# Kernel tuning notes

Hardware: AMD Instinct MI355X
Metric: run time of the kernel (lower is better)

## Reference

```python
import jax, jax.numpy as jnp
import numpy as np

B, T, M, D, K, L = 128, 50, 4, 64, 64, 16  # batch, seq len, num_beh, embed dim, num_classes, capsule_length
NUM_ITEMS = 100000
R_ITERS = 3


def _dyn_gru(x, C, Wx, bx, Wh, bh):
    """Dynamic capsule GRU. x: [B,M,T,D], C: [B,M,T,K,L] (routing state modulates update gate).
    Returns final hidden beh_e [B,M,K,L] and per-step candidate states beh_N [B,M,T,K,L]."""
    # precompute input projections for all steps: [B,M,T,3,K,L]
    gi = (jnp.einsum('bmtd,mdg->bmtg', x, Wx) + bx[:, None, :]).reshape(x.shape[0], M, T, 3, K, L)

    def step(h, inp):
        gi_t, C_t = inp  # gi_t: [B,M,3,K,L], C_t: [B,M,K,L]
        gh = (jnp.einsum('bmkl,mklg->bmkg', h, Wh) + bh).reshape(h.shape[0], M, K, 3, L)
        r = jax.nn.sigmoid(gi_t[:, :, 0] + gh[:, :, :, 0])
        z = jax.nn.sigmoid(gi_t[:, :, 1] + gh[:, :, :, 1] + C_t)  # dynamic gate via routing state C
        n = jnp.tanh(gi_t[:, :, 2] + r * gh[:, :, :, 2])
        h_new = (1.0 - z) * n + z * h
        return h_new, n

    h0 = jnp.zeros((x.shape[0], M, K, L), x.dtype)
    h_fin, ns = jax.lax.scan(step, h0, (jnp.moveaxis(gi, 2, 0), jnp.moveaxis(C, 2, 0)))
    return h_fin, jnp.moveaxis(ns, 0, 2)


def setup_inputs() -> dict:
    key = jax.random.key(0)
    ks = jax.random.split(key, 9)
    names = ['purchase_seq', 'cart_seq', 'fav_seq', 'click_seq']
    seqs = {n: jax.random.randint(k, (B, T), 0, NUM_ITEMS + 1) for n, k in zip(names, ks[:4])}
    item_emb = jax.random.normal(ks[4], (NUM_ITEMS + 1, D), jnp.float32) * 0.02
    item_emb = item_emb.at[0].set(0.0)  # padding_idx=0
    W = 0.01 * jax.random.uniform(ks[5], (K, L, M, K), jnp.float32)
    W_coef = 0.1 * jax.random.normal(ks[6], (K, D + L, L), jnp.float32)
    alpha = jnp.ones((1,), jnp.float32) * K
    w = jnp.ones((K,), jnp.float32)
    bias = jnp.zeros((K,), jnp.float32)
    gru_Wx = 0.05 * jax.random.normal(ks[7], (M, D, 3 * K * L), jnp.float32)
    gru_bx = jnp.zeros((M, 3 * K * L), jnp.float32)
    gru_Wh = 0.05 * jax.random.normal(ks[8], (M, K, L, 3 * L), jnp.float32)
    gru_bh = jnp.zeros((M, K, 3 * L), jnp.float32)
    return dict(**seqs, item_emb=item_emb, W=W, W_coef=W_coef, alpha=alpha, w=w, bias=bias,
                gru_Wx=gru_Wx, gru_bx=gru_bx, gru_Wh=gru_Wh, gru_bh=gru_bh)


def reference(purchase_seq, cart_seq, fav_seq, click_seq, item_emb, W, W_coef,
              alpha, w, bias, gru_Wx, gru_bx, gru_Wh, gru_bh):
    sg = jax.lax.stop_gradient

    def embed(seq):
        mask = (seq != 0).astype(item_emb.dtype)[..., None]
        return item_emb[seq] * mask

    x = jnp.stack([embed(purchase_seq), embed(cart_seq), embed(fav_seq), embed(click_seq)], axis=1)  # [B,M,T,D]
    bsz = x.shape[0]
    b = jnp.zeros((bsz, K, K, 1), x.dtype)
    C = jnp.zeros((bsz, M, T, K, L), x.dtype)

    # routing iterations (all GRU outputs / W / alpha / w / bias / item_emb detached; W_coef live)
    for _ in range(R_ITERS - 1):
        beh_e, beh_N = _dyn_gru(sg(x), sg(C), sg(gru_Wx), sg(gru_bx), sg(gru_Wh), sg(gru_bh))
        beh_e = sg(beh_e).transpose(0, 2, 1, 3)  # [B,K,M,L]
        u = jnp.einsum('bctd,cdtC->bcCd', beh_e, sg(W))  # [B,K,K,L]
        c = jax.nn.softmax(b, axis=2)
        v = sg(alpha) * jnp.sum(c * u, axis=1)  # [B,K,L]
        v_ = jnp.linalg.norm(v, axis=-1) * sg(w) + sg(bias)  # [B,K]
        E = sg(item_emb)
        p = jax.nn.softmax(v_ @ E.T, axis=-1) @ E  # [B,D]
        p = jnp.broadcast_to(p[:, None, :], (bsz, K, D))
        r = jnp.einsum('bcd,cdD->bcD', jnp.concatenate([p, v], axis=-1), W_coef)  # [B,K,L]
        b = b + jnp.sum(u * r[:, None], axis=-1, keepdims=True)
        C = C + sg(beh_N) * r[:, None, None]

    beh_e, _ = _dyn_gru(x, C, gru_Wx, gru_bx, gru_Wh, gru_bh)
    beh_e = beh_e.transpose(0, 2, 1, 3)
    u_hat = jnp.einsum('bctd,cdtC->bcCd', beh_e, W)
    c = jax.nn.softmax(b, axis=2)
    v = alpha * jnp.sum(c * u_hat, axis=1)
    v_ = jnp.linalg.norm(v, axis=-1) * w + bias
    return v_ @ item_emb.T  # [B, num_items+1]
```

## Files before the change

kernel.cpp:

```cpp
#include <hip/hip_runtime.h>
#include <hip/hip_bf16.h>
#include <cstdint>
#include <cstddef>

#define B_   128
#define T_   50
#define M_   4
#define D_   64
#define K_   64
#define L_   16
#define NIT  100001
#define NBP3 256
#define CHUNK3 391
#define PSTRIDE 8320

typedef unsigned short u16;
typedef unsigned int   u32;
typedef __attribute__((ext_vector_type(8))) short short8;
typedef __attribute__((ext_vector_type(4))) short short4v;
typedef __attribute__((ext_vector_type(4))) float f32x4;

__device__ __forceinline__ float bf2f(u16 v){ u32 u = ((u32)v)<<16; float f; __builtin_memcpy(&f,&u,4); return f; }
__device__ __forceinline__ u16 f2bf(float f){
  u32 u; __builtin_memcpy(&u,&f,4);
  u32 r = (u + 0x7FFFu + ((u>>16)&1u)) >> 16;
  return (u16)r;
}
__device__ __forceinline__ float fexp(float x){ return __builtin_amdgcn_exp2f(x*1.4426950408889634f); }
__device__ __forceinline__ float fsig(float x){ return __builtin_amdgcn_rcpf(1.0f + fexp(-x)); }
__device__ __forceinline__ float ftanh(float x){ return 1.0f - 2.0f*__builtin_amdgcn_rcpf(1.0f + fexp(2.0f*x)); }
__device__ __forceinline__ void unpack8(const u32* s, short8& h, short8& l){
  #pragma unroll
  for (int q=0;q<8;q++){ h[q]=(short)(s[q]&0xFFFFu); l[q]=(short)(s[q]>>16); }
}

#define MFMA32(A,Bv,C) __builtin_amdgcn_mfma_f32_16x16x32_bf16(A,Bv,C,0,0,0)

#if __has_builtin(__builtin_amdgcn_mfma_f32_16x16x16bf16_1k)
__device__ __forceinline__ f32x4 mfma16(short4v a, short4v b, f32x4 c){
  return __builtin_amdgcn_mfma_f32_16x16x16bf16_1k(a,b,c,0,0,0);
}
#elif __has_builtin(__builtin_amdgcn_mfma_f32_16x16x16_bf16)
__device__ __forceinline__ f32x4 mfma16(short4v a, short4v b, f32x4 c){
  return __builtin_amdgcn_mfma_f32_16x16x16_bf16(a,b,c,0,0,0);
}
#else
__device__ __forceinline__ f32x4 mfma16(short4v a, short4v b, f32x4 c){
  asm("v_mfma_f32_16x16x16_bf16 %0, %1, %2, %0" : "+v"(c) : "v"(a), "v"(b));
  return c;
}
#endif

__global__ __launch_bounds__(256) void k_prep_x(const int* __restrict__ s0, const int* __restrict__ s1,
  const int* __restrict__ s2, const int* __restrict__ s3, const float* __restrict__ E,
  u16* __restrict__ xh, u16* __restrict__ xl)
{
  int id = blockIdx.x*256 + threadIdx.x;
  int e8 = id & 7;
  int rm = id >> 3;
  int m = rm / 6400; int r = rm - m*6400;
  int t = r >> 7, b = r & 127;
  const int* sq = (m==0)? s0 : (m==1)? s1 : (m==2)? s2 : s3;
  int idx = sq[b*T_ + t];
  float sc = (idx==0)? 0.0f : 1.0f;
  const float4* ep = (const float4*)(E + (size_t)idx*64 + e8*8);
  float4 v0 = ep[0], v1 = ep[1];
  float vals[8] = {v0.x,v0.y,v0.z,v0.w,v1.x,v1.y,v1.z,v1.w};
  u32 hw[4], lw[4];
  #pragma unroll
  for (int q=0;q<4;q++){
    float f0 = vals[2*q]*sc, f1 = vals[2*q+1]*sc;
    u16 h0 = f2bf(f0), h1 = f2bf(f1);
    u16 l0 = f2bf(f0 - bf2f(h0)), l1 = f2bf(f1 - bf2f(h1));
    hw[q] = (u32)h0 | ((u32)h1<<16);
    lw[q] = (u32)l0 | ((u32)l1<<16);
  }
  size_t off = (size_t)rm*64 + e8*8;
  uint4 hv; hv.x=hw[0]; hv.y=hw[1]; hv.z=hw[2]; hv.w=hw[3];
  uint4 lv; lv.x=lw[0]; lv.y=lw[1]; lv.z=lw[2]; lv.w=lw[3];
  *(uint4*)(xh + off) = hv;
  *(uint4*)(xl + off) = lv;
}

__global__ __launch_bounds__(256) void k_prep_w(const float* __restrict__ Wx,
  u16* __restrict__ wh, u16* __restrict__ wl)
{
  __shared__ float tl[64][65];
  int m = blockIdx.x / 48, gt = blockIdx.x % 48;
  for (int it=0; it<16; ++it){
    int li = threadIdx.x + it*256;
    int dl = li >> 6, gl = li & 63;
    tl[dl][gl] = Wx[((size_t)m*64 + dl)*3072 + gt*64 + gl];
  }
  __syncthreads();
  for (int it=0; it<2; ++it){
    int unit = threadIdx.x + it*256;
    int gl = unit >> 3, d8 = unit & 7;
    u32 hw[4], lw[4];
    #pragma unroll
    for (int q=0;q<4;q++){
      float f0 = tl[d8*8+2*q][gl], f1 = tl[d8*8+2*q+1][gl];
      u16 h0 = f2bf(f0), h1 = f2bf(f1);
      u16 l0 = f2bf(f0 - bf2f(h0)), l1 = f2bf(f1 - bf2f(h1));
      hw[q] = (u32)h0 | ((u32)h1<<16);
      lw[q] = (u32)l0 | ((u32)l1<<16);
    }
    size_t off = ((size_t)m*3072 + gt*64 + gl)*64 + d8*8;
    uint4 hv; hv.x=hw[0]; hv.y=hw[1]; hv.z=hw[2]; hv.w=hw[3];
    uint4 lv; lv.x=lw[0]; lv.y=lw[1]; lv.z=lw[2]; lv.w=lw[3];
    *(uint4*)(wh + off) = hv;
    *(uint4*)(wl + off) = lv;
  }
}

template<int PASS>
__global__ __launch_bounds__(256,2) void k_gru_mfma(
  const u16* __restrict__ xh, const u16* __restrict__ xl,
  const u16* __restrict__ wh, const u16* __restrict__ wl,
  const float* __restrict__ Wh, const float* __restrict__ bx, const float* __restrict__ bhp,
  const float* __restrict__ rp1, const float* __restrict__ rp2,
  const u16* __restrict__ Nr1, const u16* __restrict__ Nr2,
  u16* __restrict__ Nw, float* __restrict__ behE)
{
  int tid = threadIdx.x;
  int lane = tid & 63;
  int n16 = lane & 15, quad = lane >> 4;
  int j0 = quad*4;
  int wid = blockIdx.x*4 + (tid>>6);
  int bt = wid & 7, k = (wid>>3)&63, m = wid>>9;
  int b = bt*16 + n16;

  short8 WxH[3][2], WxL[3][2];
  #pragma unroll
  for (int g=0; g<3; ++g){
    int grow = g*1024 + k*16 + n16;
    #pragma unroll
    for (int c=0; c<2; ++c){
      size_t off = ((size_t)(m*3072 + grow))*64 + c*32 + quad*8;
      WxH[g][c] = *(const short8*)(wh + off);
      WxL[g][c] = *(const short8*)(wl + off);
    }
  }
  const float* whp = Wh + ((size_t)(m*64+k)*16)*48;
  short4v WhH[3], WhL[3];
  #pragma unroll
  for (int g=0; g<3; ++g){
    short4v hhv, llv;
    #pragma unroll
    for (int i=0;i<4;i++){
      float w = whp[(j0+i)*48 + g*16 + n16];
      u16 hbits = f2bf(w);
      hhv[i] = (short)hbits;
      llv[i] = (short)f2bf(w - bf2f(hbits));
    }
    WhH[g]=hhv; WhL[g]=llv;
  }
  float biasv[3][4], bhn[4];
  #pragma unroll
  for (int g=0; g<3; ++g)
    #pragma unroll
    for (int rg=0; rg<4; ++rg){
      int j = j0+rg;
      float tb = bx[m*3072 + g*1024 + k*16 + j];
      if (g<2) tb += bhp[(m*64+k)*48 + g*16 + j];
      biasv[g][rg] = tb;
    }
  #pragma unroll
  for (int rg=0; rg<4; ++rg) bhn[rg] = bhp[(m*64+k)*48 + 32 + j0 + rg];

  float rv1[4]={0.f,0.f,0.f,0.f}, rv2[4]={0.f,0.f,0.f,0.f};
  if (PASS>=2){
    float4 q = *(const float4*)(rp1 + ((size_t)b*64+k)*16 + j0);
    rv1[0]=q.x; rv1[1]=q.y; rv1[2]=q.z; rv1[3]=q.w;
  }
  if (PASS==3){
    float4 q = *(const float4*)(rp2 + ((size_t)b*64+k)*16 + j0);
    rv2[0]=q.x; rv2[1]=q.y; rv2[2]=q.z; rv2[3]=q.w;
  }

  size_t xrow  = ((size_t)m*6400 + bt*16 + n16)*64 + quad*8;
  size_t nbase = ((size_t)(m*64+k))*102400 + (size_t)b*16 + j0;

  short4v hH = {0,0,0,0}, hL = {0,0,0,0};
  float hprev[4] = {0.f,0.f,0.f,0.f};

  short8 A0,A1,A2,A3, Bb0,Bb1,Bb2,Bb3;
  uint2 AN1={0,0}, AN2={0,0}, BN1={0,0}, BN2={0,0};

#define LOADA(tt) { size_t xo = xrow + (size_t)(tt)*8192; \
  A0 = *(const short8*)(xh + xo); A1 = *(const short8*)(xh + xo + 32); \
  A2 = *(const short8*)(xl + xo); A3 = *(const short8*)(xl + xo + 32); \
  if (PASS>=2) AN1 = *(const uint2*)(Nr1 + nbase + (size_t)(tt)*2048); \
  if (PASS==3) AN2 = *(const uint2*)(Nr2 + nbase + (size_t)(tt)*2048); }
#define LOADB(tt) { size_t xo = xrow + (size_t)(tt)*8192; \
  Bb0 = *(const short8*)(xh + xo); Bb1 = *(const short8*)(xh + xo + 32); \
  Bb2 = *(const short8*)(xl + xo); Bb3 = *(const short8*)(xl + xo + 32); \
  if (PASS>=2) BN1 = *(const uint2*)(Nr1 + nbase + (size_t)(tt)*2048); \
  if (PASS==3) BN2 = *(const uint2*)(Nr2 + nbase + (size_t)(tt)*2048); }

#define GRU_STEP(tt, X0,X1,X2,X3, NV1, NV2) { \
  f32x4 giA0 = {biasv[0][0], biasv[0][1], biasv[0][2], biasv[0][3]}; \
  f32x4 giA1 = {biasv[1][0], biasv[1][1], biasv[1][2], biasv[1][3]}; \
  f32x4 giA2 = {biasv[2][0], biasv[2][1], biasv[2][2], biasv[2][3]}; \
  giA0 = MFMA32(WxH[0][0], X0, giA0); giA1 = MFMA32(WxH[1][0], X0, giA1); giA2 = MFMA32(WxH[2][0], X0, giA2); \
  giA0 = MFMA32(WxH[0][1], X1, giA0); giA1 = MFMA32(WxH[1][1], X1, giA1); giA2 = MFMA32(WxH[2][1], X1, giA2); \
  giA0 = MFMA32(WxL[0][0], X0, giA0); giA1 = MFMA32(WxL[1][0], X0, giA1); giA2 = MFMA32(WxL[2][0], X0, giA2); \
  giA0 = MFMA32(WxL[0][1], X1, giA0); giA1 = MFMA32(WxL[1][1], X1, giA1); giA2 = MFMA32(WxL[2][1], X1, giA2); \
  giA0 = MFMA32(WxH[0][0], X2, giA0); giA1 = MFMA32(WxH[1][0], X2, giA1); giA2 = MFMA32(WxH[2][0], X2, giA2); \
  giA0 = MFMA32(WxH[0][1], X3, giA0); giA1 = MFMA32(WxH[1][1], X3, giA1); giA2 = MFMA32(WxH[2][1], X3, giA2); \
  f32x4 ghr = {0.f,0.f,0.f,0.f}, ghz = {0.f,0.f,0.f,0.f}; \
  f32x4 ghn = {bhn[0], bhn[1], bhn[2], bhn[3]}; \
  ghr = mfma16(WhH[0], hH, ghr); ghz = mfma16(WhH[1], hH, ghz); ghn = mfma16(WhH[2], hH, ghn); \
  ghr = mfma16(WhL[0], hH, ghr); ghz = mfma16(WhL[1], hH, ghz); ghn = mfma16(WhL[2], hH, ghn); \
  ghr = mfma16(WhH[0], hL, ghr); ghz = mfma16(WhH[1], hL, ghz); ghn = mfma16(WhH[2], hL, ghn); \
  u32 np0=0, np1=0; \
  short4v hHn = {0,0,0,0}, hLn = {0,0,0,0}; \
  _Pragma("unroll") \
  for (int rg=0; rg<4; ++rg){ \
    float Ct = 0.f; \
    if (PASS>=2){ u32 wb = (rg<2)? NV1.x : NV1.y; Ct = bf2f((u16)(wb >> ((rg&1)*16))) * rv1[rg]; } \
    if (PASS==3){ u32 wb = (rg<2)? NV2.x : NV2.y; Ct += bf2f((u16)(wb >> ((rg&1)*16))) * rv2[rg]; } \
    float rr = fsig(giA0[rg] + ghr[rg]); \
    float zz = fsig(giA1[rg] + ghz[rg] + Ct); \
    float nn = ftanh(giA2[rg] + rr*ghn[rg]); \
    float hvv = nn + zz*(hprev[rg]-nn); \
    hprev[rg] = hvv; \
    if (PASS<=2){ \
      u32 nb = f2bf(nn); \
      if (rg==0) np0 |= nb; else if (rg==1) np0 |= nb<<16; else if (rg==2) np1 |= nb; else np1 |= nb<<16; \
    } \
    u16 hb = f2bf(hvv); \
    hHn[rg] = (short)hb; \
    hLn[rg] = (short)f2bf(hvv - bf2f(hb)); \
  } \
  if (PASS<=2){ uint2 stv; stv.x=np0; stv.y=np1; *(uint2*)(Nw + nbase + (size_t)(tt)*2048) = stv; } \
  hH = hHn; hL = hLn; \
}

  LOADA(0);
  for (int t=0; t<48; t+=2){
    LOADB(t+1);
    GRU_STEP(t,   A0,A1,A2,A3, AN1,AN2);
    LOADA(t+2);
    GRU_STEP(t+1, Bb0,Bb1,Bb2,Bb3, BN1,BN2);
  }
  LOADB(49);
  GRU_STEP(48, A0,A1,A2,A3, AN1,AN2);
  GRU_STEP(49, Bb0,Bb1,Bb2,Bb3, BN1,BN2);
#undef GRU_STEP
#undef LOADA
#undef LOADB

  float4 stv; stv.x=hprev[0]; stv.y=hprev[1]; stv.z=hprev[2]; stv.w=hprev[3];
  *(float4*)(behE + (((size_t)b*64 + k)*4 + m)*16 + j0) = stv;
}

__global__ __launch_bounds__(256) void k_cv(const float* __restrict__ bmat, const float* __restrict__ behE,
  const float* __restrict__ W, const float* __restrict__ alpha, const float* __restrict__ wv,
  const float* __restrict__ bias, float* __restrict__ vout, float* __restrict__ vT)
{
  __shared__ float cm[64][65];
  __shared__ float vsh[64][17];
  __shared__ float besh[4096];
  int b = blockIdx.x, tid = threadIdx.x;
  for (int it=0; it<16; ++it){
    int li = tid + it*256;
    cm[li>>6][li&63] = bmat[(size_t)b*4096 + li];
    besh[li] = behE[(size_t)b*4096 + li];
  }
  __syncthreads();
  if (tid < 64){
    float mx = -1e30f;
    for (int jj=0;jj<64;jj++) mx = fmaxf(mx, cm[tid][jj]);
    float sm = 0.f;
    for (int jj=0;jj<64;jj++){ float e = fexp(cm[tid][jj]-mx); cm[tid][jj]=e; sm+=e; }
    float inv = 1.0f/sm;
    for (int jj=0;jj<64;jj++) cm[tid][jj] *= inv;
  }
  __syncthreads();
  int j = tid & 63, dq = tid>>6;
  float a0=0,a1=0,a2=0,a3=0;
  for (int i=0;i<64;++i){
    float cij = cm[i][j];
    #pragma unroll
    for (int q=0;q<4;++q){
      int d = dq*4+q;
      const float* wp = W + ((size_t)((i*16+d)*4))*64 + j;
      float uu = besh[i*64+d]*wp[0] + besh[i*64+16+d]*wp[64]
               + besh[i*64+32+d]*wp[128] + besh[i*64+48+d]*wp[192];
      float cu = cij*uu;
      if (q==0) a0 += cu; else if (q==1) a1 += cu; else if (q==2) a2 += cu; else a3 += cu;
    }
  }
  float al = alpha[0];
  a0*=al; a1*=al; a2*=al; a3*=al;
  vsh[j][dq*4]=a0; vsh[j][dq*4+1]=a1; vsh[j][dq*4+2]=a2; vsh[j][dq*4+3]=a3;
  float* vp = vout + ((size_t)b*64 + j)*16 + dq*4;
  vp[0]=a0; vp[1]=a1; vp[2]=a2; vp[3]=a3;
  __syncthreads();
  if (tid < 64){
    float s=0.f;
    #pragma unroll
    for (int dd=0; dd<16; ++dd){ float q = vsh[tid][dd]; s += q*q; }
    vT[tid*128 + b] = sqrtf(s)*wv[tid] + bias[tid];
  }
}

__global__ __launch_bounds__(256) void k_prep_v(const float* __restrict__ vT, u32* __restrict__ vBp)
{
  int id = blockIdx.x*256 + threadIdx.x;
  int b = id>>6, c = id&63;
  float v = vT[c*128 + b];
  u16 h = f2bf(v); u16 l = f2bf(v - bf2f(h));
  vBp[id] = (u32)h | ((u32)l<<16);
}

__global__ __launch_bounds__(256) void k_pfused(const u32* __restrict__ vBp, const float* __restrict__ E,
  float* __restrict__ partial)
{
  __shared__ u16 etAh[32*72], etAl[32*72];
  __shared__ u16 etBh[64*32], etBl[64*32];
  __shared__ u32 exT[128*36];
  int tid = threadIdx.x, lane = tid&63, w = tid>>6;
  int n16 = lane&15, quad = lane>>4;

  short8 vh[2][2], vl[2][2];
  #pragma unroll
  for (int nt2=0; nt2<2; ++nt2){
    int b = (2*w+nt2)*16 + n16;
    #pragma unroll
    for (int s=0; s<2; ++s){
      u32 tmp[8];
      const u32* src = vBp + b*64 + s*32 + quad*8;
      #pragma unroll
      for (int q=0;q<8;q++) tmp[q]=src[q];
      unpack8(tmp, vh[nt2][s], vl[nt2][s]);
    }
  }
  f32x4 pacc[2][4];
  #pragma unroll
  for (int a2=0;a2<2;a2++)
    #pragma unroll
    for (int b2=0;b2<4;b2++){ pacc[a2][b2][0]=0.f; pacc[a2][b2][1]=0.f; pacc[a2][b2][2]=0.f; pacc[a2][b2][3]=0.f; }
  float srun[2] = {0.f, 0.f};

  int start = blockIdx.x*CHUNK3;
  int bend = start + CHUNK3; if (bend > NIT) bend = NIT;
  int sitem = tid>>3, sc0 = (tid&7)*8;
  for (int ch=0; ch<13; ++ch){
    int i0 = start + ch*32;
    if (i0 >= bend) break;
    {
      int gidx = i0 + sitem;
      float vals[8];
      if (gidx < NIT){
        float4 a = ((const float4*)E)[(size_t)gidx*16 + (sc0>>2)];
        float4 b2 = ((const float4*)E)[(size_t)gidx*16 + (sc0>>2) + 1];
        vals[0]=a.x; vals[1]=a.y; vals[2]=a.z; vals[3]=a.w;
        vals[4]=b2.x; vals[5]=b2.y; vals[6]=b2.z; vals[7]=b2.w;
      } else {
        #pragma unroll
        for (int q=0;q<8;q++) vals[q]=0.f;
      }
      u16 hh[8], ll[8];
      #pragma unroll
      for (int q=0;q<8;q++){ hh[q]=f2bf(vals[q]); ll[q]=f2bf(vals[q]-bf2f(hh[q])); }
      *(short8*)(etAh + sitem*72 + sc0) = *(short8*)hh;
      *(short8*)(etAl + sitem*72 + sc0) = *(short8*)ll;
      #pragma unroll
      for (int q=0;q<8;q++){
        etBh[(sc0+q)*32 + sitem] = hh[q];
        etBl[(sc0+q)*32 + sitem] = ll[q];
      }
    }
    __syncthreads();
    short8 Eh[2][2], El[2][2];
    #pragma unroll
    for (int mt=0; mt<2; ++mt)
      #pragma unroll
      for (int s=0; s<2; ++s){
        Eh[mt][s] = *(const short8*)(etAh + (mt*16 + n16)*72 + s*32 + quad*8);
        El[mt][s] = *(const short8*)(etAl + (mt*16 + n16)*72 + s*32 + quad*8);
      }
    #pragma unroll
    for (int mt=0; mt<2; ++mt){
      #pragma unroll
      for (int nt2=0; nt2<2; ++nt2){
        f32x4 a = {0.f,0.f,0.f,0.f};
        #pragma unroll
        for (int s=0; s<2; ++s){
          a = __builtin_amdgcn_mfma_f32_16x16x32_bf16(Eh[mt][s], vh[nt2][s], a, 0,0,0);
          a = __builtin_amdgcn_mfma_f32_16x16x32_bf16(Eh[mt][s], vl[nt2][s], a, 0,0,0);
          a = __builtin_amdgcn_mfma_f32_16x16x32_bf16(El[mt][s], vh[nt2][s], a, 0,0,0);
        }
        u32 packed[4];
        #pragma unroll
        for (int rg=0; rg<4; ++rg){
          int it_g = i0 + mt*16 + quad*4 + rg;
          float ex = (it_g < bend)? fexp(a[rg]) : 0.f;
          srun[nt2] += ex;
          u16 h = f2bf(ex); u16 l = f2bf(ex - bf2f(h));
          packed[rg] = (u32)h | ((u32)l<<16);
        }
        int bl = (2*w+nt2)*16 + n16;
        uint4 st; st.x=packed[0]; st.y=packed[1]; st.z=packed[2]; st.w=packed[3];
        *(uint4*)(exT + bl*36 + mt*16 + quad*4) = st;
      }
    }
    __syncthreads();
    short8 Xh[2], Xl[2];
    #pragma unroll
    for (int mt2=0; mt2<2; ++mt2){
      int bl = (2*w+mt2)*16 + n16;
      uint4 t0 = *(const uint4*)(exT + bl*36 + quad*8);
      uint4 t1 = *(const uint4*)(exT + bl*36 + quad*8 + 4);
      u32 tmp[8] = {t0.x,t0.y,t0.z,t0.w,t1.x,t1.y,t1.z,t1.w};
      unpack8(tmp, Xh[mt2], Xl[mt2]);
    }
    #pragma unroll
    for (int nt3=0; nt3<4; ++nt3){
      int d = nt3*16 + n16;
      short8 Bh = *(const short8*)(etBh + d*32 + quad*8);
      short8 Bl = *(const short8*)(etBl + d*32 + quad*8);
      #pragma unroll
      for (int mt2=0; mt2<2; ++mt2){
        pacc[mt2][nt3] = __builtin_amdgcn_mfma_f32_16x16x32_bf16(Xh[mt2], Bh, pacc[mt2][nt3], 0,0,0);
        pacc[mt2][nt3] = __builtin_amdgcn_mfma_f32_16x16x32_bf16(Xh[mt2], Bl, pacc[mt2][nt3], 0,0,0);
        pacc[mt2][nt3] = __builtin_amdgcn_mfma_f32_16x16x32_bf16(Xl[mt2], Bh, pacc[mt2][nt3], 0,0,0);
      }
    }
    __syncthreads();
  }
  float* dst = partial + (size_t)blockIdx.x*PSTRIDE;
  #pragma unroll
  for (int mt2=0; mt2<2; ++mt2)
    #pragma unroll
    for (int nt3=0; nt3<4; ++nt3)
      #pragma unroll
      for (int rg=0; rg<4; ++rg){
        int b_g = (2*w+mt2)*16 + quad*4 + rg;
        int d_g = nt3*16 + n16;
        dst[b_g*64 + d_g] = pacc[mt2][nt3][rg];
      }
  #pragma unroll
  for (int nt2=0; nt2<2; ++nt2){
    float vsum = srun[nt2];
    vsum += __shfl_xor(vsum, 16);
    vsum += __shfl_xor(vsum, 32);
    if (quad == 0) dst[8192 + (2*w+nt2)*16 + n16] = vsum;
  }
}

__global__ __launch_bounds__(256) void k_pcomb(const float* __restrict__ partial, float* __restrict__ p)
{
  int id = blockIdx.x*256 + threadIdx.x;
  int b = id>>6;
  float a = 0.f, s = 0.f;
  for (int q=0;q<NBP3;q++){
    a += partial[(size_t)q*PSTRIDE + id];
    s += partial[(size_t)q*PSTRIDE + 8192 + b];
  }
  p[id] = a/s;
}

__global__ __launch_bounds__(256) void k_r(const float* __restrict__ p, const float* __restrict__ v,
  const float* __restrict__ Wc, float* __restrict__ r, float* __restrict__ rT)
{
  int gid = blockIdx.x*256 + threadIdx.x;
  int l = gid & 15, j = (gid>>4)&63, b = gid>>10;
  const float* wc = Wc + ((size_t)j*80)*16 + l;
  const float* pbp = p + b*64;
  float acc = 0.f;
  #pragma unroll 8
  for (int d=0; d<64; ++d) acc += pbp[d]*wc[d*16];
  const float* vb = v + ((size_t)b*64 + j)*16;
  #pragma unroll
  for (int d=0; d<16; ++d) acc += vb[d]*wc[(64+d)*16];
  r[((size_t)b*64+j)*16 + l] = acc;
  rT[((size_t)b*16+l)*64 + j] = acc;
}

__global__ __launch_bounds__(256) void k_bupd(const float* __restrict__ behE, const float* __restrict__ W,
  const float* __restrict__ rT, float* __restrict__ bmat)
{
  int lane = threadIdx.x & 63;
  int idx = blockIdx.x*4 + (threadIdx.x>>6);
  int b = idx >> 6, i = idx & 63;
  const float* be = behE + (size_t)idx*64;
  const float* rp = rT + (size_t)b*1024;
  float acc = 0.f;
  #pragma unroll
  for (int d=0; d<16; ++d){
    const float* wp = W + ((size_t)((i*16+d)*4))*64 + lane;
    float uu = be[d]*wp[0] + be[16+d]*wp[64] + be[32+d]*wp[128] + be[48+d]*wp[192];
    acc += uu * rp[d*64 + lane];
  }
  bmat[(size_t)idx*64 + lane] += acc;
}

__global__ __launch_bounds__(256) void k_logits(const u32* __restrict__ vBp, const float* __restrict__ E,
  float* __restrict__ out)
{
  __shared__ u16 etAh[64*72], etAl[64*72];
  __shared__ float lt[128*68];
  int tid = threadIdx.x, lane = tid&63, w = tid>>6;
  int n16 = lane&15, quad = lane>>4;
  short8 vh[2][2], vl[2][2];
  #pragma unroll
  for (int nt2=0; nt2<2; ++nt2){
    int b = (2*w+nt2)*16 + n16;
    #pragma unroll
    for (int s=0; s<2; ++s){
      u32 tmp[8];
      const u32* src = vBp + b*64 + s*32 + quad*8;
      #pragma unroll
      for (int q=0;q<8;q++) tmp[q]=src[q];
      unpack8(tmp, vh[nt2][s], vl[nt2][s]);
    }
  }
  int i0 = blockIdx.x*64;
  {
    int sitem = tid>>2, sc0 = (tid&3)*16;
    int gidx = i0 + sitem;
    float vals[16];
    if (gidx < NIT){
      #pragma unroll
      for (int q=0;q<4;q++){
        float4 a = ((const float4*)E)[(size_t)gidx*16 + (sc0>>2) + q];
        vals[4*q]=a.x; vals[4*q+1]=a.y; vals[4*q+2]=a.z; vals[4*q+3]=a.w;
      }
    } else {
      #pragma unroll
      for (int q=0;q<16;q++) vals[q]=0.f;
    }
    u16 hh[16], ll[16];
    #pragma unroll
    for (int q=0;q<16;q++){ hh[q]=f2bf(vals[q]); ll[q]=f2bf(vals[q]-bf2f(hh[q])); }
    *(short8*)(etAh + sitem*72 + sc0)     = *(short8*)hh;
    *(short8*)(etAh + sitem*72 + sc0 + 8) = *(short8*)(hh+8);
    *(short8*)(etAl + sitem*72 + sc0)     = *(short8*)ll;
    *(short8*)(etAl + sitem*72 + sc0 + 8) = *(short8*)(ll+8);
  }
  __syncthreads();
  #pragma unroll
  for (int mt=0; mt<4; ++mt){
    short8 Eh[2], El[2];
    #pragma unroll
    for (int s=0; s<2; ++s){
      Eh[s] = *(const short8*)(etAh + (mt*16 + n16)*72 + s*32 + quad*8);
      El[s] = *(const short8*)(etAl + (mt*16 + n16)*72 + s*32 + quad*8);
    }
    #pragma unroll
    for (int nt2=0; nt2<2; ++nt2){
      f32x4 a = {0.f,0.f,0.f,0.f};
      #pragma unroll
      for (int s=0; s<2; ++s){
        a = __builtin_amdgcn_mfma_f32_16x16x32_bf16(Eh[s], vh[nt2][s], a, 0,0,0);
        a = __builtin_amdgcn_mfma_f32_16x16x32_bf16(Eh[s], vl[nt2][s], a, 0,0,0);
        a = __builtin_amdgcn_mfma_f32_16x16x32_bf16(El[s], vh[nt2][s], a, 0,0,0);
      }
      int b = (2*w+nt2)*16 + n16;
      *(float4*)(lt + b*68 + mt*16 + quad*4) = *(float4*)&a;
    }
  }
  __syncthreads();
  int col = tid & 63, rgp = tid >> 6;
  if (i0 + col < NIT){
    #pragma unroll
    for (int rr=0; rr<32; ++rr){
      int b = rgp*32 + rr;
      out[(size_t)b*NIT + i0 + col] = lt[b*68 + col];
    }
  }
}

extern "C" void kernel_launch(void* const* d_in, const int* in_sizes, int n_in,
                              void* d_out, int out_size, void* d_ws, size_t ws_size,
                              hipStream_t stream)
{
  (void)in_sizes; (void)n_in; (void)out_size; (void)ws_size;
  const int*   s0 = (const int*)d_in[0];
  const int*   s1 = (const int*)d_in[1];
  const int*   s2 = (const int*)d_in[2];
  const int*   s3 = (const int*)d_in[3];
  const float* E  = (const float*)d_in[4];
  const float* W  = (const float*)d_in[5];
  const float* Wc = (const float*)d_in[6];
  const float* alpha = (const float*)d_in[7];
  const float* wv    = (const float*)d_in[8];
  const float* bias  = (const float*)d_in[9];
  const float* Wx = (const float*)d_in[10];
  const float* bx = (const float*)d_in[11];
  const float* Wh = (const float*)d_in[12];
  const float* bh = (const float*)d_in[13];

  char* ws = (char*)d_ws;
  size_t off = 0;
  auto alloc = [&](size_t bytes)->void*{ void* q = ws + off; off += (bytes + 255) & ~(size_t)255; return q; };
  u16*   N1   = (u16*)  alloc((size_t)M_*K_*T_*B_*16*2);
  u16*   N2   = (u16*)  alloc((size_t)M_*K_*T_*B_*16*2);
  u16*   xh   = (u16*)  alloc((size_t)M_*6400*64*2);
  u16*   xl   = (u16*)  alloc((size_t)M_*6400*64*2);
  u16*   wh   = (u16*)  alloc((size_t)M_*3072*64*2);
  u16*   wl   = (u16*)  alloc((size_t)M_*3072*64*2);
  float* bmat = (float*)alloc((size_t)B_*64*64*4);
  float* behE = (float*)alloc((size_t)B_*64*4*16*4);
  float* v    = (float*)alloc((size_t)B_*64*16*4);
  float* vT   = (float*)alloc((size_t)64*128*4);
  u32*   vBp  = (u32*)  alloc((size_t)128*64*4);
  float* r1   = (float*)alloc((size_t)B_*64*16*4);
  float* rT1  = (float*)alloc((size_t)B_*64*16*4);
  float* r2   = (float*)alloc((size_t)B_*64*16*4);
  float* rT2  = (float*)alloc((size_t)B_*64*16*4);
  float* p    = (float*)alloc((size_t)B_*64*4);
  float* partial = (float*)alloc((size_t)NBP3*PSTRIDE*4);

  hipMemsetAsync(bmat, 0, (size_t)B_*64*64*4, stream);
  k_prep_x<<<800,256,0,stream>>>(s0,s1,s2,s3,E,xh,xl);
  k_prep_w<<<192,256,0,stream>>>(Wx,wh,wl);

  k_gru_mfma<1><<<512,256,0,stream>>>(xh,xl,wh,wl,Wh,bx,bh,
                                      nullptr,nullptr,nullptr,nullptr, N1, behE);
  k_cv<<<128,256,0,stream>>>(bmat,behE,W,alpha,wv,bias,v,vT);
  k_prep_v<<<32,256,0,stream>>>(vT,vBp);
  k_pfused<<<NBP3,256,0,stream>>>(vBp,E,partial);
  k_pcomb<<<32,256,0,stream>>>(partial,p);
  k_r<<<512,256,0,stream>>>(p,v,Wc,r1,rT1);
  k_bupd<<<2048,256,0,stream>>>(behE,W,rT1,bmat);

  k_gru_mfma<2><<<512,256,0,stream>>>(xh,xl,wh,wl,Wh,bx,bh,
                                      r1,nullptr, N1,nullptr, N2, behE);
  k_cv<<<128,256,0,stream>>>(bmat,behE,W,alpha,wv,bias,v,vT);
  k_prep_v<<<32,256,0,stream>>>(vT,vBp);
  k_pfused<<<NBP3,256,0,stream>>>(vBp,E,partial);
  k_pcomb<<<32,256,0,stream>>>(partial,p);
  k_r<<<512,256,0,stream>>>(p,v,Wc,r2,rT2);
  k_bupd<<<2048,256,0,stream>>>(behE,W,rT2,bmat);

  k_gru_mfma<3><<<512,256,0,stream>>>(xh,xl,wh,wl,Wh,bx,bh,
                                      r1,r2, N1,N2, nullptr, behE);
  k_cv<<<128,256,0,stream>>>(bmat,behE,W,alpha,wv,bias,v,vT);
  k_prep_v<<<32,256,0,stream>>>(vT,vBp);
  k_logits<<<1563,256,0,stream>>>(vBp,E,(float*)d_out);
}
```

Measured before the change: 505.2 us.

## Software-pipeline GRU input projection one step ahead of recurrent update

Splits each GRU step into an input-projection stage (the Wx MFMAs on x_t) and a recurrent stage (the Wh MFMAs plus gate math). The projection for step t+1 is now issued before the recurrent update of step t, and loads run two steps ahead. Because the projection does not depend on the hidden state, its MFMAs can overlap the latency of the serial recurrent chain. The cost is more live accumulator registers, which may lower occupancy or cause spills.

```diff
diff --git a/kernel.cpp b/kernel.cpp
--- a/kernel.cpp
+++ b/kernel.cpp
@@ -184,72 +184,84 @@
   short4v hH = {0,0,0,0}, hL = {0,0,0,0};
   float hprev[4] = {0.f,0.f,0.f,0.f};
 
-  short8 A0,A1,A2,A3, Bb0,Bb1,Bb2,Bb3;
-  uint2 AN1={0,0}, AN2={0,0}, BN1={0,0}, BN2={0,0};
-
-#define LOADA(tt) { size_t xo = xrow + (size_t)(tt)*8192; \
-  A0 = *(const short8*)(xh + xo); A1 = *(const short8*)(xh + xo + 32); \
-  A2 = *(const short8*)(xl + xo); A3 = *(const short8*)(xl + xo + 32); \
-  if (PASS>=2) AN1 = *(const uint2*)(Nr1 + nbase + (size_t)(tt)*2048); \
-  if (PASS==3) AN2 = *(const uint2*)(Nr2 + nbase + (size_t)(tt)*2048); }
-#define LOADB(tt) { size_t xo = xrow + (size_t)(tt)*8192; \
-  Bb0 = *(const short8*)(xh + xo); Bb1 = *(const short8*)(xh + xo + 32); \
-  Bb2 = *(const short8*)(xl + xo); Bb3 = *(const short8*)(xl + xo + 32); \
-  if (PASS>=2) BN1 = *(const uint2*)(Nr1 + nbase + (size_t)(tt)*2048); \
-  if (PASS==3) BN2 = *(const uint2*)(Nr2 + nbase + (size_t)(tt)*2048); }
-
-#define GRU_STEP(tt, X0,X1,X2,X3, NV1, NV2) { \
-  f32x4 giA0 = {biasv[0][0], biasv[0][1], biasv[0][2], biasv[0][3]}; \
-  f32x4 giA1 = {biasv[1][0], biasv[1][1], biasv[1][2], biasv[1][3]}; \
-  f32x4 giA2 = {biasv[2][0], biasv[2][1], biasv[2][2], biasv[2][3]}; \
-  giA0 = MFMA32(WxH[0][0], X0, giA0); giA1 = MFMA32(WxH[1][0], X0, giA1); giA2 = MFMA32(WxH[2][0], X0, giA2); \
-  giA0 = MFMA32(WxH[0][1], X1, giA0); giA1 = MFMA32(WxH[1][1], X1, giA1); giA2 = MFMA32(WxH[2][1], X1, giA2); \
-  giA0 = MFMA32(WxL[0][0], X0, giA0); giA1 = MFMA32(WxL[1][0], X0, giA1); giA2 = MFMA32(WxL[2][0], X0, giA2); \
-  giA0 = MFMA32(WxL[0][1], X1, giA0); giA1 = MFMA32(WxL[1][1], X1, giA1); giA2 = MFMA32(WxL[2][1], X1, giA2); \
-  giA0 = MFMA32(WxH[0][0], X2, giA0); giA1 = MFMA32(WxH[1][0], X2, giA1); giA2 = MFMA32(WxH[2][0], X2, giA2); \
-  giA0 = MFMA32(WxH[0][1], X3, giA0); giA1 = MFMA32(WxH[1][1], X3, giA1); giA2 = MFMA32(WxH[2][1], X3, giA2); \
-  f32x4 ghr = {0.f,0.f,0.f,0.f}, ghz = {0.f,0.f,0.f,0.f}; \
-  f32x4 ghn = {bhn[0], bhn[1], bhn[2], bhn[3]}; \
-  ghr = mfma16(WhH[0], hH, ghr); ghz = mfma16(WhH[1], hH, ghz); ghn = mfma16(WhH[2], hH, ghn); \
-  ghr = mfma16(WhL[0], hH, ghr); ghz = mfma16(WhL[1], hH, ghz); ghn = mfma16(WhL[2], hH, ghn); \
-  ghr = mfma16(WhH[0], hL, ghr); ghz = mfma16(WhH[1], hL, ghz); ghn = mfma16(WhH[2], hL, ghn); \
-  u32 np0=0, np1=0; \
-  short4v hHn = {0,0,0,0}, hLn = {0,0,0,0}; \
-  _Pragma("unroll") \
-  for (int rg=0; rg<4; ++rg){ \
-    float Ct = 0.f; \
-    if (PASS>=2){ u32 wb = (rg<2)? NV1.x : NV1.y; Ct = bf2f((u16)(wb >> ((rg&1)*16))) * rv1[rg]; } \
-    if (PASS==3){ u32 wb = (rg<2)? NV2.x : NV2.y; Ct += bf2f((u16)(wb >> ((rg&1)*16))) * rv2[rg]; } \
-    float rr = fsig(giA0[rg] + ghr[rg]); \
-    float zz = fsig(giA1[rg] + ghz[rg] + Ct); \
-    float nn = ftanh(giA2[rg] + rr*ghn[rg]); \
-    float hvv = nn + zz*(hprev[rg]-nn); \
-    hprev[rg] = hvv; \
-    if (PASS<=2){ \
-      u32 nb = f2bf(nn); \
-      if (rg==0) np0 |= nb; else if (rg==1) np0 |= nb<<16; else if (rg==2) np1 |= nb; else np1 |= nb<<16; \
-    } \
-    u16 hb = f2bf(hvv); \
-    hHn[rg] = (short)hb; \
-    hLn[rg] = (short)f2bf(hvv - bf2f(hb)); \
-  } \
-  if (PASS<=2){ uint2 stv; stv.x=np0; stv.y=np1; *(uint2*)(Nw + nbase + (size_t)(tt)*2048) = stv; } \
-  hH = hHn; hL = hLn; \
-}
-
-  LOADA(0);
+  short8 xA0,xA1,xA2,xA3, xB0,xB1,xB2,xB3;
+  uint2 NA1={0,0}, NA2={0,0}, NB1={0,0}, NB2={0,0};
+  f32x4 gX0,gX1,gX2, gY0,gY1,gY2;
+
+  auto LXA=[&](int tt){ size_t xo=xrow+(size_t)tt*8192;
+    xA0=*(const short8*)(xh+xo); xA1=*(const short8*)(xh+xo+32);
+    xA2=*(const short8*)(xl+xo); xA3=*(const short8*)(xl+xo+32); };
+  auto LXB=[&](int tt){ size_t xo=xrow+(size_t)tt*8192;
+    xB0=*(const short8*)(xh+xo); xB1=*(const short8*)(xh+xo+32);
+    xB2=*(const short8*)(xl+xo); xB3=*(const short8*)(xl+xo+32); };
+  auto LNA=[&](int tt){
+    if(PASS>=2) NA1=*(const uint2*)(Nr1+nbase+(size_t)tt*2048);
+    if(PASS==3) NA2=*(const uint2*)(Nr2+nbase+(size_t)tt*2048); };
+  auto LNB=[&](int tt){
+    if(PASS>=2) NB1=*(const uint2*)(Nr1+nbase+(size_t)tt*2048);
+    if(PASS==3) NB2=*(const uint2*)(Nr2+nbase+(size_t)tt*2048); };
+
+  auto GI=[&](const short8&X0,const short8&X1,const short8&X2,const short8&X3,
+              f32x4&G0,f32x4&G1,f32x4&G2){
+    f32x4 a0={biasv[0][0],biasv[0][1],biasv[0][2],biasv[0][3]};
+    f32x4 a1={biasv[1][0],biasv[1][1],biasv[1][2],biasv[1][3]};
+    f32x4 a2={biasv[2][0],biasv[2][1],biasv[2][2],biasv[2][3]};
+    a0=MFMA32(WxH[0][0],X0,a0); a1=MFMA32(WxH[1][0],X0,a1); a2=MFMA32(WxH[2][0],X0,a2);
+    a0=MFMA32(WxH[0][1],X1,a0); a1=MFMA32(WxH[1][1],X1,a1); a2=MFMA32(WxH[2][1],X1,a2);
+    a0=MFMA32(WxL[0][0],X0,a0); a1=MFMA32(WxL[1][0],X0,a1); a2=MFMA32(WxL[2][0],X0,a2);
+    a0=MFMA32(WxL[0][1],X1,a0); a1=MFMA32(WxL[1][1],X1,a1); a2=MFMA32(WxL[2][1],X1,a2);
+    a0=MFMA32(WxH[0][0],X2,a0); a1=MFMA32(WxH[1][0],X2,a1); a2=MFMA32(WxH[2][0],X2,a2);
+    a0=MFMA32(WxH[0][1],X3,a0); a1=MFMA32(WxH[1][1],X3,a1); a2=MFMA32(WxH[2][1],X3,a2);
+    G0=a0; G1=a1; G2=a2;
+  };
+
+  auto STEP=[&](int tt, const f32x4&g0,const f32x4&g1,const f32x4&g2, uint2 NV1, uint2 NV2){
+    f32x4 ghr={0.f,0.f,0.f,0.f}, ghz={0.f,0.f,0.f,0.f};
+    f32x4 ghn={bhn[0],bhn[1],bhn[2],bhn[3]};
+    ghr=mfma16(WhH[0],hH,ghr); ghz=mfma16(WhH[1],hH,ghz); ghn=mfma16(WhH[2],hH,ghn);
+    ghr=mfma16(WhL[0],hH,ghr); ghz=mfma16(WhL[1],hH,ghz); ghn=mfma16(WhL[2],hH,ghn);
+    ghr=mfma16(WhH[0],hL,ghr); ghz=mfma16(WhH[1],hL,ghz); ghn=mfma16(WhH[2],hL,ghn);
+    u32 np0=0, np1=0;
+    short4v hHn={0,0,0,0}, hLn={0,0,0,0};
+    #pragma unroll
+    for(int rg=0;rg<4;++rg){
+      float Ct=0.f;
+      if(PASS>=2){ u32 wb=(rg<2)?NV1.x:NV1.y; Ct = bf2f((u16)(wb>>((rg&1)*16)))*rv1[rg]; }
+      if(PASS==3){ u32 wb=(rg<2)?NV2.x:NV2.y; Ct += bf2f((u16)(wb>>((rg&1)*16)))*rv2[rg]; }
+      float rr=fsig(g0[rg]+ghr[rg]);
+      float zz=fsig(g1[rg]+ghz[rg]+Ct);
+      float nn=ftanh(g2[rg]+rr*ghn[rg]);
+      float hvv=nn+zz*(hprev[rg]-nn);
+      hprev[rg]=hvv;
+      if(PASS<=2){
+        u32 nb=f2bf(nn);
+        if(rg==0)np0|=nb; else if(rg==1)np0|=nb<<16; else if(rg==2)np1|=nb; else np1|=nb<<16;
+      }
+      u16 hb=f2bf(hvv);
+      hHn[rg]=(short)hb;
+      hLn[rg]=(short)f2bf(hvv-bf2f(hb));
+    }
+    if(PASS<=2){ uint2 stv; stv.x=np0; stv.y=np1; *(uint2*)(Nw+nbase+(size_t)tt*2048)=stv; }
+    hH=hHn; hL=hLn;
+  };
+
+  LXA(0); LNA(0);
+  LXB(1); LNB(1);
+  GI(xA0,xA1,xA2,xA3, gX0,gX1,gX2);
+
   for (int t=0; t<48; t+=2){
-    LOADB(t+1);
-    GRU_STEP(t,   A0,A1,A2,A3, AN1,AN2);
-    LOADA(t+2);
-    GRU_STEP(t+1, Bb0,Bb1,Bb2,Bb3, BN1,BN2);
-  }
-  LOADB(49);
-  GRU_STEP(48, A0,A1,A2,A3, AN1,AN2);
-  GRU_STEP(49, Bb0,Bb1,Bb2,Bb3, BN1,BN2);
-#undef GRU_STEP
-#undef LOADA
-#undef LOADB
+    LXA(t+2);
+    GI(xB0,xB1,xB2,xB3, gY0,gY1,gY2);
+    STEP(t, gX0,gX1,gX2, NA1,NA2);
+    LNA(t+2);
+    LXB(t+3);
+    GI(xA0,xA1,xA2,xA3, gX0,gX1,gX2);
+    STEP(t+1, gY0,gY1,gY2, NB1,NB2);
+    LNB(t+3);
+  }
+  GI(xB0,xB1,xB2,xB3, gY0,gY1,gY2);
+  STEP(48, gX0,gX1,gX2, NA1,NA2);
+  STEP(49, gY0,gY1,gY2, NB1,NB2);
 
   float4 stv; stv.x=hprev[0]; stv.y=hprev[1]; stv.z=hprev[2]; stv.w=hprev[3];
   *(float4*)(behE + (((size_t)b*64 + k)*4 + m)*16 + j0) = stv;
```

After: 501.2 us. Within noise of the previous version (-0.8%).

## Pack recurrent GRU matmul into K=32 MFMAs and fuse v bf16 packing into k_cv

Applied to the files above, without the earlier changes.

The hidden-state recurrent product used nine 16x16x16 MFMAs per step for the split-bf16 terms (hi*hi, lo*hi, hi*lo). The new code packs Wh hi/lo into one short8 operand and rebuilds the hidden-state B operand with ds_bpermute lane shuffles, so the same terms fit in six 16x16x32 MFMAs on the serial critical path. The lo*lo term is zeroed by masking. Separately, k_prep_v is removed and its hi/lo packing is folded into k_cv, which drops three kernel launches and the vT round trip. The bpermute shuffles add LDS-path latency to each recurrent step.

```diff
diff --git a/kernel.cpp b/kernel.cpp
--- a/kernel.cpp
+++ b/kernel.cpp
@@ -17,7 +17,6 @@
 typedef unsigned short u16;
 typedef unsigned int   u32;
 typedef __attribute__((ext_vector_type(8))) short short8;
-typedef __attribute__((ext_vector_type(4))) short short4v;
 typedef __attribute__((ext_vector_type(4))) float f32x4;
 
 __device__ __forceinline__ float bf2f(u16 v){ u32 u = ((u32)v)<<16; float f; __builtin_memcpy(&f,&u,4); return f; }
@@ -29,27 +28,15 @@
 __device__ __forceinline__ float fexp(float x){ return __builtin_amdgcn_exp2f(x*1.4426950408889634f); }
 __device__ __forceinline__ float fsig(float x){ return __builtin_amdgcn_rcpf(1.0f + fexp(-x)); }
 __device__ __forceinline__ float ftanh(float x){ return 1.0f - 2.0f*__builtin_amdgcn_rcpf(1.0f + fexp(2.0f*x)); }
+__device__ __forceinline__ u32 bperm(int idx, u32 v){
+  return (u32)__builtin_amdgcn_ds_bpermute(idx, (int)v);
+}
 __device__ __forceinline__ void unpack8(const u32* s, short8& h, short8& l){
   #pragma unroll
   for (int q=0;q<8;q++){ h[q]=(short)(s[q]&0xFFFFu); l[q]=(short)(s[q]>>16); }
 }
 
 #define MFMA32(A,Bv,C) __builtin_amdgcn_mfma_f32_16x16x32_bf16(A,Bv,C,0,0,0)
-
-#if __has_builtin(__builtin_amdgcn_mfma_f32_16x16x16bf16_1k)
-__device__ __forceinline__ f32x4 mfma16(short4v a, short4v b, f32x4 c){
-  return __builtin_amdgcn_mfma_f32_16x16x16bf16_1k(a,b,c,0,0,0);
-}
-#elif __has_builtin(__builtin_amdgcn_mfma_f32_16x16x16_bf16)
-__device__ __forceinline__ f32x4 mfma16(short4v a, short4v b, f32x4 c){
-  return __builtin_amdgcn_mfma_f32_16x16x16_bf16(a,b,c,0,0,0);
-}
-#else
-__device__ __forceinline__ f32x4 mfma16(short4v a, short4v b, f32x4 c){
-  asm("v_mfma_f32_16x16x16_bf16 %0, %1, %2, %0" : "+v"(c) : "v"(a), "v"(b));
-  return c;
-}
-#endif
 
 __global__ __launch_bounds__(256) void k_prep_x(const int* __restrict__ s0, const int* __restrict__ s1,
   const int* __restrict__ s2, const int* __restrict__ s3, const float* __restrict__ E,
@@ -142,18 +129,18 @@
     }
   }
   const float* whp = Wh + ((size_t)(m*64+k)*16)*48;
-  short4v WhH[3], WhL[3];
+  short8 WhP[3];
   #pragma unroll
   for (int g=0; g<3; ++g){
-    short4v hhv, llv;
-    #pragma unroll
-    for (int i=0;i<4;i++){
-      float w = whp[(j0+i)*48 + g*16 + n16];
-      u16 hbits = f2bf(w);
-      hhv[i] = (short)hbits;
-      llv[i] = (short)f2bf(w - bf2f(hbits));
-    }
-    WhH[g]=hhv; WhL[g]=llv;
+    short8 p;
+    #pragma unroll
+    for (int e=0; e<8; ++e){
+      int l = ((quad & 1) ? 8 : 0) + e;
+      float w = whp[l*48 + g*16 + n16];
+      u16 hb = f2bf(w);
+      p[e] = (quad < 2) ? (short)hb : (short)f2bf(w - bf2f(hb));
+    }
+    WhP[g] = p;
   }
   float biasv[3][4], bhn[4];
   #pragma unroll
@@ -181,7 +168,11 @@
   size_t xrow  = ((size_t)m*6400 + bt*16 + n16)*64 + quad*8;
   size_t nbase = ((size_t)(m*64+k))*102400 + (size_t)b*16 + j0;
 
-  short4v hH = {0,0,0,0}, hL = {0,0,0,0};
+  int idxlo = (((lane & 15) | ((lane & 16) << 1)) << 2);
+  int idxhi = idxlo + 64;
+  u32 zmask = (lane < 32) ? 0xFFFFFFFFu : 0u;
+
+  short8 B1 = {0,0,0,0,0,0,0,0}, B2 = {0,0,0,0,0,0,0,0};
   float hprev[4] = {0.f,0.f,0.f,0.f};
 
   short8 A0,A1,A2,A3, Bb0,Bb1,Bb2,Bb3;
@@ -210,11 +201,9 @@
   giA0 = MFMA32(WxH[0][1], X3, giA0); giA1 = MFMA32(WxH[1][1], X3, giA1); giA2 = MFMA32(WxH[2][1], X3, giA2); \
   f32x4 ghr = {0.f,0.f,0.f,0.f}, ghz = {0.f,0.f,0.f,0.f}; \
   f32x4 ghn = {bhn[0], bhn[1], bhn[2], bhn[3]}; \
-  ghr = mfma16(WhH[0], hH, ghr); ghz = mfma16(WhH[1], hH, ghz); ghn = mfma16(WhH[2], hH, ghn); \
-  ghr = mfma16(WhL[0], hH, ghr); ghz = mfma16(WhL[1], hH, ghz); ghn = mfma16(WhL[2], hH, ghn); \
-  ghr = mfma16(WhH[0], hL, ghr); ghz = mfma16(WhH[1], hL, ghz); ghn = mfma16(WhH[2], hL, ghn); \
-  u32 np0=0, np1=0; \
-  short4v hHn = {0,0,0,0}, hLn = {0,0,0,0}; \
+  ghr = MFMA32(WhP[0], B1, ghr); ghz = MFMA32(WhP[1], B1, ghz); ghn = MFMA32(WhP[2], B1, ghn); \
+  ghr = MFMA32(WhP[0], B2, ghr); ghz = MFMA32(WhP[1], B2, ghz); ghn = MFMA32(WhP[2], B2, ghn); \
+  u32 np0=0, np1=0, hw0=0, hw1=0, lw0=0, lw1=0; \
   _Pragma("unroll") \
   for (int rg=0; rg<4; ++rg){ \
     float Ct = 0.f; \
@@ -229,12 +218,22 @@
       u32 nb = f2bf(nn); \
       if (rg==0) np0 |= nb; else if (rg==1) np0 |= nb<<16; else if (rg==2) np1 |= nb; else np1 |= nb<<16; \
     } \
-    u16 hb = f2bf(hvv); \
-    hHn[rg] = (short)hb; \
-    hLn[rg] = (short)f2bf(hvv - bf2f(hb)); \
+    u32 hb = f2bf(hvv); \
+    u32 lb = f2bf(hvv - bf2f((u16)hb)); \
+    if (rg==0){ hw0 |= hb; lw0 |= lb; } \
+    else if (rg==1){ hw0 |= hb<<16; lw0 |= lb<<16; } \
+    else if (rg==2){ hw1 |= hb; lw1 |= lb; } \
+    else { hw1 |= hb<<16; lw1 |= lb<<16; } \
   } \
   if (PASS<=2){ uint2 stv; stv.x=np0; stv.y=np1; *(uint2*)(Nw + nbase + (size_t)(tt)*2048) = stv; } \
-  hH = hHn; hL = hLn; \
+  u32 g0 = bperm(idxlo, hw0), g1 = bperm(idxlo, hw1); \
+  u32 g2 = bperm(idxhi, hw0), g3 = bperm(idxhi, hw1); \
+  u32 c0 = bperm(idxlo, lw0) & zmask, c1 = bperm(idxlo, lw1) & zmask; \
+  u32 c2 = bperm(idxhi, lw0) & zmask, c3 = bperm(idxhi, lw1) & zmask; \
+  union { u32 w[4]; short8 s; } uB1, uB2; \
+  uB1.w[0]=g0; uB1.w[1]=g1; uB1.w[2]=g2; uB1.w[3]=g3; \
+  uB2.w[0]=c0; uB2.w[1]=c1; uB2.w[2]=c2; uB2.w[3]=c3; \
+  B1 = uB1.s; B2 = uB2.s; \
 }
 
   LOADA(0);
@@ -257,7 +256,7 @@
 
 __global__ __launch_bounds__(256) void k_cv(const float* __restrict__ bmat, const float* __restrict__ behE,
   const float* __restrict__ W, const float* __restrict__ alpha, const float* __restrict__ wv,
-  const float* __restrict__ bias, float* __restrict__ vout, float* __restrict__ vT)
+  const float* __restrict__ bias, float* __restrict__ vout, u32* __restrict__ vBp)
 {
   __shared__ float cm[64][65];
   __shared__ float vsh[64][17];
@@ -302,17 +301,10 @@
     float s=0.f;
     #pragma unroll
     for (int dd=0; dd<16; ++dd){ float q = vsh[tid][dd]; s += q*q; }
-    vT[tid*128 + b] = sqrtf(s)*wv[tid] + bias[tid];
-  }
-}
-
-__global__ __launch_bounds__(256) void k_prep_v(const float* __restrict__ vT, u32* __restrict__ vBp)
-{
-  int id = blockIdx.x*256 + threadIdx.x;
-  int b = id>>6, c = id&63;
-  float v = vT[c*128 + b];
-  u16 h = f2bf(v); u16 l = f2bf(v - bf2f(h));
-  vBp[id] = (u32)h | ((u32)l<<16);
+    float val = sqrtf(s)*wv[tid] + bias[tid];
+    u16 h = f2bf(val); u16 l = f2bf(val - bf2f(h));
+    vBp[b*64 + tid] = (u32)h | ((u32)l<<16);
+  }
 }
 
 __global__ __launch_bounds__(256) void k_pfused(const u32* __restrict__ vBp, const float* __restrict__ E,
@@ -606,7 +598,6 @@
   float* bmat = (float*)alloc((size_t)B_*64*64*4);
   float* behE = (float*)alloc((size_t)B_*64*4*16*4);
   float* v    = (float*)alloc((size_t)B_*64*16*4);
-  float* vT   = (float*)alloc((size_t)64*128*4);
   u32*   vBp  = (u32*)  alloc((size_t)128*64*4);
   float* r1   = (float*)alloc((size_t)B_*64*16*4);
   float* rT1  = (float*)alloc((size_t)B_*64*16*4);
@@ -621,8 +612,7 @@
 
   k_gru_mfma<1><<<512,256,0,stream>>>(xh,xl,wh,wl,Wh,bx,bh,
                                       nullptr,nullptr,nullptr,nullptr, N1, behE);
-  k_cv<<<128,256,0,stream>>>(bmat,behE,W,alpha,wv,bias,v,vT);
-  k_prep_v<<<32,256,0,stream>>>(vT,vBp);
+  k_cv<<<128,256,0,stream>>>(bmat,behE,W,alpha,wv,bias,v,vBp);
   k_pfused<<<NBP3,256,0,stream>>>(vBp,E,partial);
   k_pcomb<<<32,256,0,stream>>>(partial,p);
   k_r<<<512,256,0,stream>>>(p,v,Wc,r1,rT1);
@@ -630,8 +620,7 @@
 
   k_gru_mfma<2><<<512,256,0,stream>>>(xh,xl,wh,wl,Wh,bx,bh,
                                       r1,nullptr, N1,nullptr, N2, behE);
-  k_cv<<<128,256,0,stream>>>(bmat,behE,W,alpha,wv,bias,v,vT);
-  k_prep_v<<<32,256,0,stream>>>(vT,vBp);
+  k_cv<<<128,256,0,stream>>>(bmat,behE,W,alpha,wv,bias,v,vBp);
   k_pfused<<<NBP3,256,0,stream>>>(vBp,E,partial);
   k_pcomb<<<32,256,0,stream>>>(partial,p);
   k_r<<<512,256,0,stream>>>(p,v,Wc,r2,rT2);
@@ -639,7 +628,6 @@
 
   k_gru_mfma<3><<<512,256,0,stream>>>(xh,xl,wh,wl,Wh,bx,bh,
                                       r1,r2, N1,N2, nullptr, behE);
-  k_cv<<<128,256,0,stream>>>(bmat,behE,W,alpha,wv,bias,v,vT);
-  k_prep_v<<<32,256,0,stream>>>(vT,vBp);
+  k_cv<<<128,256,0,stream>>>(bmat,behE,W,alpha,wv,bias,v,vBp);
   k_logits<<<1563,256,0,stream>>>(vBp,E,(float*)d_out);
 }
```

Result: slower. 518.0 us (+2.5%).
